# Performance work log

Measured on AMD Instinct MI355X. Metric: run time of the kernel, lower is better.

Reference implementation:

```python
import jax, jax.numpy as jnp
import numpy as np

N_FEAT = 64      # number of continuous features
N_BINS = 255     # bin edges per feature (EBM default) -> 256 score slots incl. OOV
N_PAIRS = 32     # interaction terms
BATCH = 262144


def _bin_indices(edges, x):
    """TF Discretization (searchsorted right) + IntegerLookup(vocab=range(B), OOV->0).
    edges: [N, B] sorted per row; x: [batch, N] -> int32 [batch, N] in [0, B]."""
    idx = jax.vmap(lambda e, col: jnp.searchsorted(e, col, side='right'),
                   in_axes=(0, 1), out_axes=1)(edges, x)  # [batch, N], values 0..B
    B = edges.shape[1]
    # IntegerLookup: value v in {0..B-1} -> v+1 ; value B (not in vocab) -> OOV index 0
    return jnp.where(idx < B, idx + 1, 0)


def setup_inputs() -> dict:
    key = jax.random.key(0)
    ks = jax.random.split(key, 6)
    x = jax.random.normal(ks[0], (BATCH, N_FEAT), dtype=jnp.float32)
    edges = jnp.sort(jax.random.normal(ks[1], (N_FEAT, N_BINS), dtype=jnp.float32), axis=1)
    pair_edges = jnp.sort(jax.random.normal(ks[2], (N_FEAT, N_BINS), dtype=jnp.float32), axis=1)
    w = jax.random.normal(ks[3], (N_FEAT, N_BINS + 1), dtype=jnp.float32) * 0.1
    tables = jax.random.normal(ks[4], (N_PAIRS, N_BINS + 1, N_BINS + 1), dtype=jnp.float32) * 0.1
    pairs = jax.random.randint(ks[5], (N_PAIRS, 2), 0, N_FEAT, dtype=jnp.int32)
    bias = jnp.zeros((1,), dtype=jnp.float32)
    return {"x": x, "edges": edges, "w": w, "pair_edges": pair_edges,
            "pairs": pairs, "tables": tables, "bias": bias}


def reference(x, edges, w, pair_edges, pairs, tables, bias):
    # --- per-feature main effects: one_hot(idx) @ Dense(1) == gather w[f, idx] ---
    idx = _bin_indices(edges, x)                                  # [batch, N]
    feat = w[jnp.arange(N_FEAT)[None, :], idx]                    # [batch, N]
    # --- pairwise interactions: gather_nd on [L, R] lookup tables ---
    pidx = _bin_indices(pair_edges, x)                            # [batch, N]
    li = pidx[:, pairs[:, 0]]                                     # [batch, P]
    ri = pidx[:, pairs[:, 1]]                                     # [batch, P]
    inter = tables[jnp.arange(N_PAIRS)[None, :], li, ri]          # [batch, P]
    # --- BiasLayer: reduce_sum(concat, axis=1) + bias, then sigmoid ---
    logits = jnp.sum(feat, axis=1) + jnp.sum(inter, axis=1) + bias[0]
    return jax.nn.sigmoid(logits)                                  # [batch]
```

## Files before the change

kernel.cpp:

```cpp
#include <hip/hip_runtime.h>
#include <hip/hip_fp16.h>

#define NBINS 255
#define NPAIRS 32
#define BIGF 3.0e38f


__global__ void ebm_prep_edges(const float* __restrict__ edges,
                               const float* __restrict__ pair_edges,
                               const float* __restrict__ w,
                               float* __restrict__ ws) {
    int tid = blockIdx.x * blockDim.x + threadIdx.x;
    float* E   = ws;
    float* PE  = ws + 16384;
    __half* W  = (__half*)(ws + 32768);
    int f = tid >> 8, j = tid & 255;
    E[tid]  = (j < NBINS) ? edges[f * NBINS + j]      : BIGF;
    PE[tid] = (j < NBINS) ? pair_edges[f * NBINS + j] : BIGF;
    int src = (j < 255) ? j + 1 : 0;
    W[tid]  = __float2half(w[f * 256 + src]);
}

__global__ void ebm_prep_tables(const float* __restrict__ tables,
                                unsigned short* __restrict__ o) {
    int i = blockIdx.x * blockDim.x + threadIdx.x;
    int b = i & 255, a = (i >> 8) & 255, p = i >> 16;
    int ra = (a < 255) ? a + 1 : 0;
    int rb = (b < 255) ? b + 1 : 0;
    float v = tables[(p << 16) + (ra << 8) + rb];
    o[i] = __half_as_ushort(__float2half(v));
}

__device__ __forceinline__ float merge2(float a, float b, int mask, int lane) {
    bool lo = (lane & mask) == 0;
    float send = lo ? b : a;
    float recv = __shfl_xor(send, mask, 64);
    float keep = lo ? a : b;
    return keep + recv;
}

__global__ __launch_bounds__(1024, 4) void ebm_main(
    const float* __restrict__ x,
    const int*   __restrict__ pairs,
    const float* __restrict__ tables_f32,
    const float* __restrict__ bias,
    const float* __restrict__ ws,
    const __half* __restrict__ T16,
    int useT16,
    float*       __restrict__ out) {

    __shared__ float  sE[16384];
    __shared__ float  sPE[16384];
    __shared__ __half sW[16384];

    const float* E  = ws;
    const float* PE = ws + 16384;
    const unsigned int* W32 = (const unsigned int*)(ws + 32768);

    int tid  = threadIdx.x;
    int lane = tid & 63;

    for (int i = tid; i < 16384; i += 1024) {
        int f = i >> 8, k = i & 255;
        sE[(f << 8) + (k ^ f)]  = E[i];
        sPE[(f << 8) + (k ^ f)] = PE[i];
    }
    {
        unsigned int* sW32 = (unsigned int*)sW;
        for (int i = tid; i < 8192; i += 1024) sW32[i] = W32[i];
    }

    float cu[15], cp[15];
#pragma unroll
    for (int j = 0; j < 15; ++j) {
        cu[j] = E[lane * 256 + 16 * j + 15];
        cp[j] = PE[lane * 256 + 16 * j + 15];
    }

    int pa = 0, pb = 0;
    if (lane < NPAIRS) { pa = pairs[2 * lane]; pb = pairs[2 * lane + 1]; }
    bool act = false;
#pragma unroll 1
    for (int k = 0; k < 2 * NPAIRS; ++k) act = act || (pairs[k] == lane);
    float bias0 = bias[0];

    __syncthreads();

    const int fbase = lane << 8;
    const int fh    = lane & 48;
    const int ci0   = 3  ^ (lane & 15);
    const int ci1   = 7  ^ (lane & 15);
    const int ci2   = 11 ^ (lane & 15);
    const int fq    = lane >> 2;

    const float4* sE4  = (const float4*)sE;
    const float4* sPE4 = (const float4*)sPE;

    int gw = blockIdx.x * 16 + (tid >> 6);
    int row0 = gw * 32;

    float xv[4];
#pragma unroll
    for (int u = 0; u < 4; ++u) xv[u] = x[(row0 + u) * 64 + lane];

#pragma unroll 1
    for (int it = 0; it < 8; ++it) {
        int rowbase = row0 + it * 4;

        float xn[4];
        int nb = (it < 7) ? (rowbase + 4) : rowbase;
#pragma unroll
        for (int u = 0; u < 4; ++u) xn[u] = x[(nb + u) * 64 + lane];

        int t[4];
#pragma unroll
        for (int u = 0; u < 4; ++u) {
            int tt = 0;
#pragma unroll
            for (int j = 0; j < 15; ++j) tt += (xv[u] >= cu[j]);
            t[u] = tt;
        }
        float ma[4][3];
#pragma unroll
        for (int u = 0; u < 4; ++u) {
            int tb = fbase + ((t[u] << 4) ^ fh);
            ma[u][0] = sE[tb + ci0];
            ma[u][1] = sE[tb + ci1];
            ma[u][2] = sE[tb + ci2];
        }

        int t2[4] = {0, 0, 0, 0};
        if (act) {
#pragma unroll
            for (int u = 0; u < 4; ++u) {
                int tt = 0;
#pragma unroll
                for (int j = 0; j < 15; ++j) tt += (xv[u] >= cp[j]);
                t2[u] = tt;
            }
        }

        int cpart[4];
        float4 fv[4];
#pragma unroll
        for (int u = 0; u < 4; ++u) {
            int m = (xv[u] >= ma[u][0]) + (xv[u] >= ma[u][1]) + (xv[u] >= ma[u][2]);
            cpart[u] = (t[u] << 4) + (m << 2);
            fv[u] = sE4[(lane << 6) + (((t[u] << 2) + m) ^ fq)];
        }

        float mb[4][3];
        if (act) {
#pragma unroll
            for (int u = 0; u < 4; ++u) {
                int tb = fbase + ((t2[u] << 4) ^ fh);
                mb[u][0] = sPE[tb + ci0];
                mb[u][1] = sPE[tb + ci1];
                mb[u][2] = sPE[tb + ci2];
            }
        }

        float wv[4];
#pragma unroll
        for (int u = 0; u < 4; ++u) {
            int cnt = (xv[u] >= fv[u].x) + (xv[u] >= fv[u].y) +
                      (xv[u] >= fv[u].z) + (xv[u] >= fv[u].w);
            int c = cpart[u] + cnt;
            wv[u] = __half2float(sW[fbase + c]);
        }

        int pidx[4] = {0, 0, 0, 0};
        if (act) {
            float4 gv[4];
#pragma unroll
            for (int u = 0; u < 4; ++u) {
                int m = (xv[u] >= mb[u][0]) + (xv[u] >= mb[u][1]) + (xv[u] >= mb[u][2]);
                pidx[u] = (t2[u] << 4) + (m << 2);
                gv[u] = sPE4[(lane << 6) + (((t2[u] << 2) + m) ^ fq)];
            }
#pragma unroll
            for (int u = 0; u < 4; ++u) {
                pidx[u] += (xv[u] >= gv[u].x) + (xv[u] >= gv[u].y) +
                           (xv[u] >= gv[u].z) + (xv[u] >= gv[u].w);
            }
        }

        int pk = pidx[0] | (pidx[1] << 8) | (pidx[2] << 16) | (pidx[3] << 24);
        int lk = __shfl(pk, pa, 64);
        int rk = __shfl(pk, pb, 64);
        float tv[4] = {0.f, 0.f, 0.f, 0.f};
        if (lane < NPAIRS) {
            if (useT16) {
#pragma unroll
                for (int u = 0; u < 4; ++u) {
                    int li = (lk >> (8 * u)) & 255;
                    int ri = (rk >> (8 * u)) & 255;
                    tv[u] = __half2float(T16[(lane << 16) + (li << 8) + ri]);
                }
            } else {
#pragma unroll
                for (int u = 0; u < 4; ++u) {
                    int li = (lk >> (8 * u)) & 255;
                    int ri = (rk >> (8 * u)) & 255;
                    int lb = (li < 255) ? li + 1 : 0;
                    int rb = (ri < 255) ? ri + 1 : 0;
                    tv[u] = tables_f32[(lane << 16) + (lb << 8) + rb];
                }
            }
        }

        float s0 = wv[0] + tv[0];
        float s1 = wv[1] + tv[1];
        float s2 = wv[2] + tv[2];
        float s3 = wv[3] + tv[3];
        float m01 = merge2(s0, s1, 1, lane);
        float m23 = merge2(s2, s3, 1, lane);
        float q   = merge2(m01, m23, 2, lane);
#pragma unroll
        for (int o = 4; o <= 32; o <<= 1) q += __shfl_xor(q, o, 64);

        if (lane < 4) {
            out[rowbase + lane] = 1.0f / (1.0f + __expf(-(q + bias0)));
        }

        xv[0] = xn[0]; xv[1] = xn[1]; xv[2] = xn[2]; xv[3] = xn[3];
    }
}

extern "C" void kernel_launch(void* const* d_in, const int* in_sizes, int n_in,
                              void* d_out, int out_size, void* d_ws, size_t ws_size,
                              hipStream_t stream) {
    const float* x          = (const float*)d_in[0];
    const float* edges      = (const float*)d_in[1];
    const float* w          = (const float*)d_in[2];
    const float* pair_edges = (const float*)d_in[3];
    const int*   pairs      = (const int*)d_in[4];
    const float* tables     = (const float*)d_in[5];
    const float* bias       = (const float*)d_in[6];
    float* out = (float*)d_out;
    float* ws  = (float*)d_ws;

    int useT16 = (ws_size >= (size_t)4358144) ? 1 : 0;
    __half* T16 = (__half*)((char*)d_ws + 163840);

    ebm_prep_edges<<<64, 256, 0, stream>>>(edges, pair_edges, w, ws);
    if (useT16) {
        ebm_prep_tables<<<2048, 1024, 0, stream>>>(tables, (unsigned short*)T16);
    }
    ebm_main<<<512, 1024, 0, stream>>>(x, pairs, tables, bias, ws, T16, useT16, out);
}
```

Baseline: 216.2 us.

## Process 8 rows per iteration and issue pair-table gathers before main-effect lookups

Widens each wave's per-iteration batch from 4 to 8 rows, halving the loop trip count and the cross-lane reduction count per row. It also reorders the work so the pair bin search and global table gathers come first, letting the main-effect shared-memory lookups overlap the global gather latency. The larger live state raises register pressure, which under the 1024-thread launch bound could cause spills or lower occupancy.

```diff
diff --git a/kernel.cpp b/kernel.cpp
--- a/kernel.cpp
+++ b/kernel.cpp
@@ -99,131 +99,140 @@
     int gw = blockIdx.x * 16 + (tid >> 6);
     int row0 = gw * 32;
 
-    float xv[4];
-#pragma unroll
-    for (int u = 0; u < 4; ++u) xv[u] = x[(row0 + u) * 64 + lane];
+    float xv[8];
+#pragma unroll
+    for (int u = 0; u < 8; ++u) xv[u] = x[(row0 + u) * 64 + lane];
 
 #pragma unroll 1
-    for (int it = 0; it < 8; ++it) {
-        int rowbase = row0 + it * 4;
-
-        float xn[4];
-        int nb = (it < 7) ? (rowbase + 4) : rowbase;
-#pragma unroll
-        for (int u = 0; u < 4; ++u) xn[u] = x[(nb + u) * 64 + lane];
-
-        int t[4];
-#pragma unroll
-        for (int u = 0; u < 4; ++u) {
+    for (int it = 0; it < 4; ++it) {
+        int rowbase = row0 + it * 8;
+
+        float xn[8];
+        int nb = (it < 3) ? (rowbase + 8) : rowbase;
+#pragma unroll
+        for (int u = 0; u < 8; ++u) xn[u] = x[(nb + u) * 64 + lane];
+
+        int pidx[8] = {0, 0, 0, 0, 0, 0, 0, 0};
+        if (act) {
+            int t2[8];
+#pragma unroll
+            for (int u = 0; u < 8; ++u) {
+                int tt = 0;
+#pragma unroll
+                for (int j = 0; j < 15; ++j) tt += (xv[u] >= cp[j]);
+                t2[u] = tt;
+            }
+            float mb[8][3];
+#pragma unroll
+            for (int u = 0; u < 8; ++u) {
+                int tb = fbase + ((t2[u] << 4) ^ fh);
+                mb[u][0] = sPE[tb + ci0];
+                mb[u][1] = sPE[tb + ci1];
+                mb[u][2] = sPE[tb + ci2];
+            }
+            float4 gv[8];
+#pragma unroll
+            for (int u = 0; u < 8; ++u) {
+                int m = (xv[u] >= mb[u][0]) + (xv[u] >= mb[u][1]) + (xv[u] >= mb[u][2]);
+                pidx[u] = (t2[u] << 4) + (m << 2);
+                gv[u] = sPE4[(lane << 6) + (((t2[u] << 2) + m) ^ fq)];
+            }
+#pragma unroll
+            for (int u = 0; u < 8; ++u) {
+                pidx[u] += (xv[u] >= gv[u].x) + (xv[u] >= gv[u].y) +
+                           (xv[u] >= gv[u].z) + (xv[u] >= gv[u].w);
+            }
+        }
+
+        int pk0 = pidx[0] | (pidx[1] << 8) | (pidx[2] << 16) | (pidx[3] << 24);
+        int pk1 = pidx[4] | (pidx[5] << 8) | (pidx[6] << 16) | (pidx[7] << 24);
+        int lk0 = __shfl(pk0, pa, 64), lk1 = __shfl(pk1, pa, 64);
+        int rk0 = __shfl(pk0, pb, 64), rk1 = __shfl(pk1, pb, 64);
+
+        float tv[8] = {0.f, 0.f, 0.f, 0.f, 0.f, 0.f, 0.f, 0.f};
+        if (lane < NPAIRS) {
+            if (useT16) {
+#pragma unroll
+                for (int u = 0; u < 4; ++u) {
+                    int li = (lk0 >> (8 * u)) & 255, ri = (rk0 >> (8 * u)) & 255;
+                    tv[u] = __half2float(T16[(lane << 16) + (li << 8) + ri]);
+                }
+#pragma unroll
+                for (int u = 0; u < 4; ++u) {
+                    int li = (lk1 >> (8 * u)) & 255, ri = (rk1 >> (8 * u)) & 255;
+                    tv[4 + u] = __half2float(T16[(lane << 16) + (li << 8) + ri]);
+                }
+            } else {
+#pragma unroll
+                for (int u = 0; u < 4; ++u) {
+                    int li = (lk0 >> (8 * u)) & 255, ri = (rk0 >> (8 * u)) & 255;
+                    int lb = (li < 255) ? li + 1 : 0, rb = (ri < 255) ? ri + 1 : 0;
+                    tv[u] = tables_f32[(lane << 16) + (lb << 8) + rb];
+                }
+#pragma unroll
+                for (int u = 0; u < 4; ++u) {
+                    int li = (lk1 >> (8 * u)) & 255, ri = (rk1 >> (8 * u)) & 255;
+                    int lb = (li < 255) ? li + 1 : 0, rb = (ri < 255) ? ri + 1 : 0;
+                    tv[4 + u] = tables_f32[(lane << 16) + (lb << 8) + rb];
+                }
+            }
+        }
+
+        int t[8];
+#pragma unroll
+        for (int u = 0; u < 8; ++u) {
             int tt = 0;
 #pragma unroll
             for (int j = 0; j < 15; ++j) tt += (xv[u] >= cu[j]);
             t[u] = tt;
         }
-        float ma[4][3];
-#pragma unroll
-        for (int u = 0; u < 4; ++u) {
+        float ma[8][3];
+#pragma unroll
+        for (int u = 0; u < 8; ++u) {
             int tb = fbase + ((t[u] << 4) ^ fh);
             ma[u][0] = sE[tb + ci0];
             ma[u][1] = sE[tb + ci1];
             ma[u][2] = sE[tb + ci2];
         }
-
-        int t2[4] = {0, 0, 0, 0};
-        if (act) {
-#pragma unroll
-            for (int u = 0; u < 4; ++u) {
-                int tt = 0;
-#pragma unroll
-                for (int j = 0; j < 15; ++j) tt += (xv[u] >= cp[j]);
-                t2[u] = tt;
-            }
-        }
-
-        int cpart[4];
-        float4 fv[4];
-#pragma unroll
-        for (int u = 0; u < 4; ++u) {
+        int cpart[8];
+        float4 fv[8];
+#pragma unroll
+        for (int u = 0; u < 8; ++u) {
             int m = (xv[u] >= ma[u][0]) + (xv[u] >= ma[u][1]) + (xv[u] >= ma[u][2]);
             cpart[u] = (t[u] << 4) + (m << 2);
             fv[u] = sE4[(lane << 6) + (((t[u] << 2) + m) ^ fq)];
         }
-
-        float mb[4][3];
-        if (act) {
-#pragma unroll
-            for (int u = 0; u < 4; ++u) {
-                int tb = fbase + ((t2[u] << 4) ^ fh);
-                mb[u][0] = sPE[tb + ci0];
-                mb[u][1] = sPE[tb + ci1];
-                mb[u][2] = sPE[tb + ci2];
-            }
-        }
-
-        float wv[4];
-#pragma unroll
-        for (int u = 0; u < 4; ++u) {
+        float wv[8];
+#pragma unroll
+        for (int u = 0; u < 8; ++u) {
             int cnt = (xv[u] >= fv[u].x) + (xv[u] >= fv[u].y) +
                       (xv[u] >= fv[u].z) + (xv[u] >= fv[u].w);
             int c = cpart[u] + cnt;
             wv[u] = __half2float(sW[fbase + c]);
         }
 
-        int pidx[4] = {0, 0, 0, 0};
-        if (act) {
-            float4 gv[4];
-#pragma unroll
-            for (int u = 0; u < 4; ++u) {
-                int m = (xv[u] >= mb[u][0]) + (xv[u] >= mb[u][1]) + (xv[u] >= mb[u][2]);
-                pidx[u] = (t2[u] << 4) + (m << 2);
-                gv[u] = sPE4[(lane << 6) + (((t2[u] << 2) + m) ^ fq)];
-            }
-#pragma unroll
-            for (int u = 0; u < 4; ++u) {
-                pidx[u] += (xv[u] >= gv[u].x) + (xv[u] >= gv[u].y) +
-                           (xv[u] >= gv[u].z) + (xv[u] >= gv[u].w);
-            }
-        }
-
-        int pk = pidx[0] | (pidx[1] << 8) | (pidx[2] << 16) | (pidx[3] << 24);
-        int lk = __shfl(pk, pa, 64);
-        int rk = __shfl(pk, pb, 64);
-        float tv[4] = {0.f, 0.f, 0.f, 0.f};
-        if (lane < NPAIRS) {
-            if (useT16) {
-#pragma unroll
-                for (int u = 0; u < 4; ++u) {
-                    int li = (lk >> (8 * u)) & 255;
-                    int ri = (rk >> (8 * u)) & 255;
-                    tv[u] = __half2float(T16[(lane << 16) + (li << 8) + ri]);
-                }
-            } else {
-#pragma unroll
-                for (int u = 0; u < 4; ++u) {
-                    int li = (lk >> (8 * u)) & 255;
-                    int ri = (rk >> (8 * u)) & 255;
-                    int lb = (li < 255) ? li + 1 : 0;
-                    int rb = (ri < 255) ? ri + 1 : 0;
-                    tv[u] = tables_f32[(lane << 16) + (lb << 8) + rb];
-                }
-            }
-        }
-
-        float s0 = wv[0] + tv[0];
-        float s1 = wv[1] + tv[1];
-        float s2 = wv[2] + tv[2];
-        float s3 = wv[3] + tv[3];
+        float s0 = wv[0] + tv[0], s1 = wv[1] + tv[1];
+        float s2 = wv[2] + tv[2], s3 = wv[3] + tv[3];
+        float s4 = wv[4] + tv[4], s5 = wv[5] + tv[5];
+        float s6 = wv[6] + tv[6], s7 = wv[7] + tv[7];
+
         float m01 = merge2(s0, s1, 1, lane);
         float m23 = merge2(s2, s3, 1, lane);
-        float q   = merge2(m01, m23, 2, lane);
-#pragma unroll
-        for (int o = 4; o <= 32; o <<= 1) q += __shfl_xor(q, o, 64);
-
-        if (lane < 4) {
-            out[rowbase + lane] = 1.0f / (1.0f + __expf(-(q + bias0)));
-        }
-
-        xv[0] = xn[0]; xv[1] = xn[1]; xv[2] = xn[2]; xv[3] = xn[3];
+        float m45 = merge2(s4, s5, 1, lane);
+        float m67 = merge2(s6, s7, 1, lane);
+        float q0  = merge2(m01, m23, 2, lane);
+        float q1  = merge2(m45, m67, 2, lane);
+        float z   = merge2(q0, q1, 4, lane);
+        z += __shfl_xor(z, 8, 64);
+        z += __shfl_xor(z, 16, 64);
+        z += __shfl_xor(z, 32, 64);
+
+        if (lane < 8) {
+            out[rowbase + lane] = 1.0f / (1.0f + __expf(-(z + bias0)));
+        }
+
+#pragma unroll
+        for (int u = 0; u < 8; ++u) xv[u] = xn[u];
     }
 }
 
```

Result: no change. 218.3 us (+1.0%).
